# Optimization experiments

Measured on AMD Instinct MI355X. Metric: run time of the kernel, lower is better.

## Reference

```python
import math
import jax, jax.numpy as jnp
import numpy as np

D_MODEL = 1024
NHEAD = 16
NUM_TEMP = 4
HEAD = D_MODEL // NHEAD          # 64
DIM = HEAD // NUM_TEMP           # 16
SCALE = math.sqrt(HEAD)
B, L = 2, 2048


def _make_freq():
    # freq = 10000^(-arange(0,dim,2)/dim), repeat_interleave(2) -> length DIM
    f = np.power(10000.0, -np.arange(0, DIM, 2) / DIM)
    return jnp.asarray(np.repeat(f, 2), dtype=jnp.float32)  # (DIM,)


def setup_inputs() -> dict:
    key = jax.random.key(0)
    ks = jax.random.split(key, 8)
    s = 0.02
    return {
        "data": jax.random.normal(ks[0], (B, L, D_MODEL), jnp.float32),
        "temporal": jax.random.uniform(ks[1], (B, L, NUM_TEMP), jnp.float32),
        "mask": jnp.zeros((L, L), jnp.float32),
        "Wq": jax.random.normal(ks[2], (D_MODEL, D_MODEL), jnp.float32) * s,
        "bq": jnp.zeros((D_MODEL,), jnp.float32),
        "Wk": jax.random.normal(ks[3], (D_MODEL, D_MODEL), jnp.float32) * s,
        "bk": jnp.zeros((D_MODEL,), jnp.float32),
        "Wv": jax.random.normal(ks[4], (D_MODEL, D_MODEL), jnp.float32) * s,
        "bv": jnp.zeros((D_MODEL,), jnp.float32),
    }


def _rotate_half_pairs(x):
    # [-x2, x1, -x4, x3, ...] along last dim
    stacked = jnp.stack([-x[..., 1::2], x[..., 0::2]], axis=-1)
    return stacked.reshape(x.shape)


def _apply_rotary(x, sine, cosine):
    # x: (B,L,H,HEAD); sine/cosine: (B,L,HEAD)
    return x * cosine[:, :, None, :] + _rotate_half_pairs(x) * sine[:, :, None, :]


def reference(data, temporal, mask, Wq, bq, Wk, bk, Wv, bv):
    freq = _make_freq()  # (DIM,)
    b, l, _ = data.shape
    q = (data @ Wq + bq).reshape(b, l, NHEAD, HEAD)
    k = (data @ Wk + bk).reshape(b, l, NHEAD, HEAD)
    v = (data @ Wv + bv).reshape(b, l, NHEAD, HEAD)
    # per-temporal-column frequencies: (B,L,T,DIM) -> (B,L,HEAD)
    freqs = (temporal[..., None] * freq).reshape(b, l, HEAD)
    cosine = jnp.cos(freqs)
    sine = jnp.sin(freqs)
    rq = _apply_rotary(q, sine, cosine)
    rk = _apply_rotary(k, sine, cosine)
    logits = jnp.einsum("bqhs,bkhs->bhqk", rq, rk) / SCALE + mask
    weights = jax.nn.softmax(logits, axis=-1)  # dropout is identity at eval
    context = jnp.einsum("bhqk,bkhs->bqhs", weights, v)
    return context.reshape(b, l, D_MODEL)
```

## Files before the change

### kernel.cpp

```cpp
#include <hip/hip_runtime.h>
#include <hip/hip_bf16.h>

#define LSEQ 2048
#define DM   1024
#define NH   16

typedef __attribute__((ext_vector_type(8)))  short bf16x8;
typedef __attribute__((ext_vector_type(8)))  unsigned short u16x8;
typedef __attribute__((ext_vector_type(4)))  float f32x4;
typedef __attribute__((ext_vector_type(16))) float f32x16;
typedef __attribute__((ext_vector_type(4)))  unsigned int u32x4;

#define LOG2E 1.4426950408889634f
#define C1SC  0.18033688011112042f
#define DEFER_THR 8.0f

static __device__ __forceinline__ float exp2fast(float x) {
  return __builtin_amdgcn_exp2f(x);
}

static __device__ __forceinline__ unsigned short f2bf(float f) {
  unsigned int u = __float_as_uint(f);
  u += 0x7FFFu + ((u >> 16) & 1u);
  return (unsigned short)(u >> 16);
}

static __device__ __forceinline__ unsigned pk2(float a, float b) {
  __hip_bfloat162 t = __float22bfloat162_rn(make_float2(a, b));
  return *reinterpret_cast<unsigned*>(&t);
}

static __device__ __forceinline__ f32x16 unpack16(u16x8 a, u16x8 b) {
  const u32x4 ua = __builtin_bit_cast(u32x4, a);
  const u32x4 ub = __builtin_bit_cast(u32x4, b);
  f32x16 r;
#pragma unroll
  for (int i = 0; i < 4; ++i) {
    r[2 * i]     = __uint_as_float(ua[i] << 16);
    r[2 * i + 1] = __uint_as_float(ua[i] & 0xFFFF0000u);
    r[8 + 2 * i]     = __uint_as_float(ub[i] << 16);
    r[8 + 2 * i + 1] = __uint_as_float(ub[i] & 0xFFFF0000u);
  }
  return r;
}

static __device__ __forceinline__ bf16x8 mkfrag(int hi, float p0, float p1,
                                                float p2, float p3, float p4,
                                                float p5, float p6, float p7) {
  unsigned w0 = pk2(p0, p1), w1 = pk2(p2, p3);
  unsigned w2 = pk2(p4, p5), w3 = pk2(p6, p7);
  unsigned s0 = hi ? w0 : w2, s1 = hi ? w1 : w3;
  unsigned t0 = __shfl_xor(s0, 32, 64);
  unsigned t1 = __shfl_xor(s1, 32, 64);
  u32x4 f;
  f[0] = hi ? t0 : w0;
  f[1] = hi ? t1 : w1;
  f[2] = hi ? w2 : t0;
  f[3] = hi ? w3 : t1;
  return __builtin_bit_cast(bf16x8, f);
}

static __device__ __forceinline__ void gld_lds16(const unsigned short* g, unsigned short* l) {
  __builtin_amdgcn_global_load_lds(
      (const __attribute__((address_space(1))) unsigned int*)g,
      (__attribute__((address_space(3))) unsigned int*)l, 16, 0, 0);
}

__global__ void k_convert_data(const float* __restrict__ src,
                               unsigned short* __restrict__ dst, int n4) {
  int i = blockIdx.x * 256 + threadIdx.x;
  if (i >= n4) return;
  float4 v = reinterpret_cast<const float4*>(src)[i];
  ushort4 o;
  o.x = f2bf(v.x); o.y = f2bf(v.y); o.z = f2bf(v.z); o.w = f2bf(v.w);
  reinterpret_cast<ushort4*>(dst)[i] = o;
}

__global__ void k_transpose_w(const float* __restrict__ Wq,
                              const float* __restrict__ Wk,
                              const float* __restrict__ Wv,
                              unsigned short* __restrict__ Wt) {
  __shared__ unsigned short tile[64][65];
  const float* W = (blockIdx.z == 0) ? Wq : (blockIdx.z == 1) ? Wk : Wv;
  int n0 = blockIdx.x * 64, k0 = blockIdx.y * 64;
  int t = threadIdx.x;
  int c = t & 63, r0 = t >> 6;
  for (int i = 0; i < 16; ++i) {
    int r = r0 + i * 4;
    tile[r][c] = f2bf(W[(size_t)(k0 + r) * DM + n0 + c]);
  }
  __syncthreads();
  size_t nbase = (size_t)blockIdx.z * DM + n0;
  for (int i = 0; i < 16; ++i) {
    int n = r0 + i * 4;
    Wt[(nbase + n) * DM + k0 + c] = tile[c][n];
  }
}

__global__ void k_maskC(const float* __restrict__ mask,
                        unsigned short* __restrict__ maskCb) {
  __shared__ float tile[64][65];
  int q0 = blockIdx.x * 64, kv0 = blockIdx.y * 64;
  int t = threadIdx.x;
  int c = t & 63, r0 = t >> 6;
  for (int i = 0; i < 16; ++i) {
    int r = r0 + i * 4;
    tile[r][c] = mask[(size_t)(q0 + r) * LSEQ + kv0 + c];
  }
  __syncthreads();
  const int q = t & 63, slot = t >> 6;
  const int tt = slot >> 1, hh = slot & 1;
  u16x8 va, vb;
#pragma unroll
  for (int r = 0; r < 8; ++r) {
    const int kvloc = 32 * tt + 4 * hh + (r & 3) + 8 * (r >> 2);
    va[r] = f2bf(tile[q][kvloc] * LOG2E);
  }
#pragma unroll
  for (int r = 8; r < 16; ++r) {
    const int kvloc = 32 * tt + 4 * hh + (r & 3) + 8 * (r >> 2);
    vb[r - 8] = f2bf(tile[q][kvloc] * LOG2E);
  }
  unsigned short* dst = maskCb + ((size_t)((kv0 >> 6) * 4 + slot) * 2048 + q0 + q) * 16;
  *reinterpret_cast<u16x8*>(dst) = va;
  *reinterpret_cast<u16x8*>(dst + 8) = vb;
}

__global__ __launch_bounds__(256) void k_qkv_gemm(
    const unsigned short* __restrict__ A, const unsigned short* __restrict__ Bt,
    const float* __restrict__ bq, const float* __restrict__ bk,
    const float* __restrict__ bv, const float* __restrict__ temporal,
    unsigned short* __restrict__ qbuf, unsigned short* __restrict__ kbuf,
    unsigned short* __restrict__ vtbuf) {
  __shared__ unsigned short As[128 * 32];
  __shared__ unsigned short Bs[128 * 32];
  __shared__ unsigned short otile[128 * 136];
  const int tid = threadIdx.x;
  const int lane = tid & 63, wid = tid >> 6;
  const int wm = wid >> 1, wn = wid & 1;
  const int lr = lane & 15, lg = lane >> 4;

  const int bid = blockIdx.x;
  const int xcd = bid & 7, rr = bid >> 3;
  const int mblk = xcd * 4 + (rr / 24);
  const int nblk = rr % 24;
  const int m0 = mblk * 128;
  const int n0 = nblk * 128;

  f32x4 acc[4][4] = {};

  const int e0 = tid * 8;
  const int e1 = (256 + tid) * 8;
  const int ra0 = e0 >> 5, ca0 = e0 & 31;
  const int ra1 = e1 >> 5, ca1 = e1 & 31;
  unsigned short* lA0 = As + wid * 512;
  unsigned short* lA1 = As + 2048 + wid * 512;
  unsigned short* lB0 = Bs + wid * 512;
  unsigned short* lB1 = Bs + 2048 + wid * 512;

  for (int k0 = 0; k0 < DM; k0 += 32) {
    __syncthreads();
    gld_lds16(A + (size_t)(m0 + ra0) * DM + k0 + ca0, lA0);
    gld_lds16(A + (size_t)(m0 + ra1) * DM + k0 + ca1, lA1);
    gld_lds16(Bt + (size_t)(n0 + ra0) * DM + k0 + ca0, lB0);
    gld_lds16(Bt + (size_t)(n0 + ra1) * DM + k0 + ca1, lB1);
    __syncthreads();
    bf16x8 af[4], bfv[4];
    for (int mi = 0; mi < 4; ++mi)
      af[mi] = *reinterpret_cast<const bf16x8*>(As + (wm * 64 + mi * 16 + lr) * 32 + lg * 8);
    for (int ni = 0; ni < 4; ++ni)
      bfv[ni] = *reinterpret_cast<const bf16x8*>(Bs + (wn * 64 + ni * 16 + lr) * 32 + lg * 8);
    for (int mi = 0; mi < 4; ++mi)
      for (int ni = 0; ni < 4; ++ni)
        acc[mi][ni] = __builtin_amdgcn_mfma_f32_16x16x32_bf16(af[mi], bfv[ni], acc[mi][ni], 0, 0, 0);
  }

  const int mat = n0 >> 10;
  const int c0 = n0 & 1023;
  const int bb = m0 >> 11;
  const int mloc = m0 & 2047;
  const float qscale = (mat == 0) ? C1SC : 1.f;

  for (int mi = 0; mi < 4; ++mi) {
    const int rrel_base = wm * 64 + mi * 16 + lg * 4;
    for (int ni = 0; ni < 4; ++ni) {
      const int crel = wn * 64 + ni * 16 + lr;
      const int c = (c0 + crel);
      const int d = c & 63;
      const float bias = (mat == 0 ? bq : mat == 1 ? bk : bv)[c];
      f32x4 v = acc[mi][ni];
      if (mat < 2) {
        const int jj = d & 15, tt = d >> 4;
        const float fr = __expf(-(float)(jj & 14) * 0.5756462732485115f);
        const float sign = (d & 1) ? 1.f : -1.f;
        for (int j = 0; j < 4; ++j) {
          const int rrel = rrel_base + j;
          const float x = v[j] + bias;
          const float part = __shfl_xor(x, 1, 64);
          const int lqs = mloc + rrel;
          const float fq = temporal[((size_t)bb * LSEQ + lqs) * 4 + tt] * fr;
          float sn, cs;
          __sincosf(fq, &sn, &cs);
          otile[rrel * 136 + crel] = f2bf((x * cs + sign * part * sn) * qscale);
        }
      } else {
        for (int j = 0; j < 4; ++j) {
          const int rrel = rrel_base + j;
          otile[crel * 136 + rrel] = f2bf(v[j] + bias);
        }
      }
    }
  }
  __syncthreads();

  for (int i = 0; i < 2; ++i) {
    const int h = (c0 >> 6) + i;
    const size_t bh = (size_t)(bb * NH + h);
    if (mat == 0) {
      const size_t base = (bh * LSEQ + mloc) * 64;
#pragma unroll
      for (int kk2 = 0; kk2 < 4; ++kk2) {
        const int e = kk2 * 2048 + tid * 8;
        const int r = e >> 6, d = e & 63;
        *reinterpret_cast<u16x8*>(qbuf + base + e) =
            *reinterpret_cast<const u16x8*>(otile + r * 136 + i * 64 + d);
      }
    } else if (mat == 1) {
      const size_t base = bh * 131072 + (size_t)(mloc >> 5) * 2048;
#pragma unroll
      for (int kk2 = 0; kk2 < 4; ++kk2) {
        const int e = kk2 * 2048 + tid * 8;
        const int r = kk2 * 32 + ((tid >> 1) & 31);
        const int d = ((tid >> 6) & 3) * 16 + (tid & 1) * 8;
        *reinterpret_cast<u16x8*>(kbuf + base + e) =
            *reinterpret_cast<const u16x8*>(otile + r * 136 + i * 64 + d);
      }
    } else {
      const size_t base = bh * 131072 + (size_t)(mloc >> 4) * 1024;
#pragma unroll
      for (int kk2 = 0; kk2 < 4; ++kk2) {
        const int e = kk2 * 2048 + tid * 8;
        const int d = ((tid >> 6) & 1) * 32 + ((tid >> 1) & 31);
        const int r = (kk2 * 2 + (tid >> 7)) * 16 + (tid & 1) * 8;
        *reinterpret_cast<u16x8*>(vtbuf + base + e) =
            *reinterpret_cast<const u16x8*>(otile + (i * 64 + d) * 136 + r);
      }
    }
  }
}

__global__ __launch_bounds__(256) void k_attn(
    const unsigned short* __restrict__ qbuf, const unsigned short* __restrict__ kbuf,
    const unsigned short* __restrict__ vtbuf, const unsigned short* __restrict__ maskCb,
    float* __restrict__ out) {
  __shared__ float otile[4][64][33];
  __shared__ float mlbuf[4][32][2];
  const int tid = threadIdx.x, lane = tid & 63, wid = tid >> 6;
  const int lq = lane & 31, hi = lane >> 5;
  const int qsub = wid & 1, kvh = wid >> 1;
  const int bh = blockIdx.y;
  const int q0 = blockIdx.x * 64 + qsub * 32;
  const int qg = q0 + lq;
  const size_t bhL = (size_t)bh * LSEQ;
  const unsigned short* kb = kbuf + (size_t)bh * 131072;
  const unsigned short* vb = vtbuf + (size_t)bh * 131072;
  const unsigned short* mb = maskCb + ((size_t)hi * 2048 + qg) * 16;

  bf16x8 qf[4];
#pragma unroll
  for (int c = 0; c < 4; ++c)
    qf[c] = *reinterpret_cast<const bf16x8*>(qbuf + (bhL + qg) * 64 + c * 16 + hi * 8);

  f32x16 o0 = {}, o1 = {};
  float m2 = -1e30f, l_run = 0.f;

  const int kv_beg = kvh * 1024, kv_end = kv_beg + 1024;
  for (int kv0 = kv_beg; kv0 < kv_end; kv0 += 64) {
    const unsigned short* mt = mb + (size_t)(kv0 >> 6) * (4 * 2048 * 16);
    f32x16 s0 = unpack16(*reinterpret_cast<const u16x8*>(mt),
                         *reinterpret_cast<const u16x8*>(mt + 8));
    f32x16 s1 = unpack16(*reinterpret_cast<const u16x8*>(mt + 2 * 2048 * 16),
                         *reinterpret_cast<const u16x8*>(mt + 2 * 2048 * 16 + 8));

    const unsigned short* kch = kb + (size_t)(kv0 >> 5) * 2048;
#pragma unroll
    for (int c = 0; c < 4; ++c) {
      bf16x8 k0 = *reinterpret_cast<const bf16x8*>(kch + c * 512 + lq * 16 + hi * 8);
      bf16x8 k1 = *reinterpret_cast<const bf16x8*>(kch + 2048 + c * 512 + lq * 16 + hi * 8);
      s0 = __builtin_amdgcn_mfma_f32_32x32x16_bf16(k0, qf[c], s0, 0, 0, 0);
      s1 = __builtin_amdgcn_mfma_f32_32x32x16_bf16(k1, qf[c], s1, 0, 0, 0);
    }

    float t0[8];
#pragma unroll
    for (int r = 0; r < 8; ++r) t0[r] = fmaxf(fmaxf(s0[r], s0[r + 8]), fmaxf(s1[r], s1[r + 8]));
#pragma unroll
    for (int r = 0; r < 4; ++r) t0[r] = fmaxf(t0[r], t0[r + 4]);
    float loc = fmaxf(fmaxf(t0[0], t0[1]), fmaxf(t0[2], t0[3]));
    loc = fmaxf(loc, __shfl_xor(loc, 32, 64));

    if (!__all(loc <= m2 + DEFER_THR)) {
      const float mn = fmaxf(m2, loc);
      const float al = exp2fast(m2 - mn);
      l_run *= al;
#pragma unroll
      for (int r = 0; r < 16; ++r) { o0[r] *= al; o1[r] *= al; }
      m2 = mn;
    }

    float rs0 = 0.f, rs1 = 0.f, rs2 = 0.f, rs3 = 0.f;
#pragma unroll
    for (int r = 0; r < 4; ++r) {
      s0[r] = exp2fast(s0[r] - m2);      rs0 += s0[r];
      s0[r + 4] = exp2fast(s0[r + 4] - m2);  rs1 += s0[r + 4];
      s0[r + 8] = exp2fast(s0[r + 8] - m2);  rs2 += s0[r + 8];
      s0[r + 12] = exp2fast(s0[r + 12] - m2); rs3 += s0[r + 12];
    }
#pragma unroll
    for (int r = 0; r < 4; ++r) {
      s1[r] = exp2fast(s1[r] - m2);      rs0 += s1[r];
      s1[r + 4] = exp2fast(s1[r + 4] - m2);  rs1 += s1[r + 4];
      s1[r + 8] = exp2fast(s1[r + 8] - m2);  rs2 += s1[r + 8];
      s1[r + 12] = exp2fast(s1[r + 12] - m2); rs3 += s1[r + 12];
    }
    float rs = (rs0 + rs1) + (rs2 + rs3);
    rs += __shfl_xor(rs, 32, 64);
    l_run += rs;

    bf16x8 pf0 = mkfrag(hi, s0[0], s0[1], s0[2], s0[3], s0[4], s0[5], s0[6], s0[7]);
    bf16x8 pf1 = mkfrag(hi, s0[8], s0[9], s0[10], s0[11], s0[12], s0[13], s0[14], s0[15]);
    bf16x8 pf2 = mkfrag(hi, s1[0], s1[1], s1[2], s1[3], s1[4], s1[5], s1[6], s1[7]);
    bf16x8 pf3 = mkfrag(hi, s1[8], s1[9], s1[10], s1[11], s1[12], s1[13], s1[14], s1[15]);

    const unsigned short* vch = vb + (size_t)(kv0 >> 4) * 1024;
#pragma unroll
    for (int ks = 0; ks < 4; ++ks) {
      bf16x8 pf = (ks == 0) ? pf0 : (ks == 1) ? pf1 : (ks == 2) ? pf2 : pf3;
      bf16x8 v0 = *reinterpret_cast<const bf16x8*>(vch + ks * 1024 + lq * 16 + hi * 8);
      bf16x8 v1 = *reinterpret_cast<const bf16x8*>(vch + ks * 1024 + 512 + lq * 16 + hi * 8);
      o0 = __builtin_amdgcn_mfma_f32_32x32x16_bf16(v0, pf, o0, 0, 0, 0);
      o1 = __builtin_amdgcn_mfma_f32_32x32x16_bf16(v1, pf, o1, 0, 0, 0);
    }
  }

  if (lane < 32) { mlbuf[wid][lq][0] = m2; mlbuf[wid][lq][1] = l_run; }
  __syncthreads();
  const int pw = wid ^ 2;
  const float m_p = mlbuf[pw][lq][0];
  const float l_p = mlbuf[pw][lq][1];
  const float mstar = fmaxf(m2, m_p);
  const float f  = exp2fast(m2 - mstar);
  const float fp = exp2fast(m_p - mstar);
  const float scale = f / (l_run * f + l_p * fp);

#pragma unroll
  for (int r = 0; r < 16; ++r) {
    const int d = (r & 3) + 8 * (r >> 2) + 4 * hi;
    otile[wid][d][lq] = o0[r] * scale;
    otile[wid][32 + d][lq] = o1[r] * scale;
  }
  __syncthreads();

  const int b = bh >> 4, h = bh & 15;
#pragma unroll
  for (int i = 0; i < 4; ++i) {
    const int u = i * 256 + tid;
    const int q = u >> 4, c4 = u & 15;
    const int qs = q >> 5, ql = q & 31;
    float4 w;
    w.x = otile[qs][c4 * 4 + 0][ql] + otile[2 + qs][c4 * 4 + 0][ql];
    w.y = otile[qs][c4 * 4 + 1][ql] + otile[2 + qs][c4 * 4 + 1][ql];
    w.z = otile[qs][c4 * 4 + 2][ql] + otile[2 + qs][c4 * 4 + 2][ql];
    w.w = otile[qs][c4 * 4 + 3][ql] + otile[2 + qs][c4 * 4 + 3][ql];
    *reinterpret_cast<float4*>(
        out + ((size_t)(b * LSEQ + blockIdx.x * 64 + q)) * DM + h * 64 + c4 * 4) = w;
  }
}

extern "C" void kernel_launch(void* const* d_in, const int* in_sizes, int n_in,
                              void* d_out, int out_size, void* d_ws, size_t ws_size,
                              hipStream_t stream) {
  const float* data     = (const float*)d_in[0];
  const float* temporal = (const float*)d_in[1];
  const float* mask     = (const float*)d_in[2];
  const float* Wq       = (const float*)d_in[3];
  const float* bq       = (const float*)d_in[4];
  const float* Wk       = (const float*)d_in[5];
  const float* bk       = (const float*)d_in[6];
  const float* Wv       = (const float*)d_in[7];
  const float* bv       = (const float*)d_in[8];
  float* out = (float*)d_out;

  char* ws = (char*)d_ws;
  unsigned short* data_bf = (unsigned short*)(ws);
  unsigned short* wt      = (unsigned short*)(ws + (size_t)8  * 1048576);
  unsigned short* qbuf    = (unsigned short*)(ws + (size_t)14 * 1048576);
  unsigned short* kbuf    = (unsigned short*)(ws + (size_t)22 * 1048576);
  unsigned short* vtbuf   = (unsigned short*)(ws + (size_t)30 * 1048576);
  unsigned short* maskCb  = data_bf;

  hipLaunchKernelGGL(k_convert_data, dim3(4096), dim3(256), 0, stream,
                     data, data_bf, (2 * LSEQ * DM) / 4);
  hipLaunchKernelGGL(k_transpose_w, dim3(16, 16, 3), dim3(256), 0, stream,
                     Wq, Wk, Wv, wt);
  hipLaunchKernelGGL(k_qkv_gemm, dim3(768), dim3(256), 0, stream,
                     data_bf, wt, bq, bk, bv, temporal, qbuf, kbuf, vtbuf);
  hipLaunchKernelGGL(k_maskC, dim3(32, 32), dim3(256), 0, stream,
                     mask, maskCb);
  hipLaunchKernelGGL(k_attn, dim3(32, 32), dim3(256), 0, stream,
                     qbuf, kbuf, vtbuf, maskCb, out);
}
```

Before: 140.3 us.

## Replace online-softmax max tracking with fixed offset and overflow rescale, skip zero mask tiles

Removes the per-tile row-max reduction and deferred rescale from the attention loop. Softmax now uses a fixed initial offset and rescales by 2^-12 only when a row's partial exp sum exceeds a threshold. The mask kernel also writes per-tile all-zero flags so attention can skip loading mask tiles that are zero. Separately, the P fragments are packed without the cross-lane shuffle, which implies a changed V^T layout and gather in the QKV epilogue. This relies on logits being bounded, since a very negative max could underflow and a large jump in one tile could overflow before the rescale check fires.

```diff
diff --git a/kernel.cpp b/kernel.cpp
--- a/kernel.cpp
+++ b/kernel.cpp
@@ -13,7 +13,6 @@
 
 #define LOG2E 1.4426950408889634f
 #define C1SC  0.18033688011112042f
-#define DEFER_THR 8.0f
 
 static __device__ __forceinline__ float exp2fast(float x) {
   return __builtin_amdgcn_exp2f(x);
@@ -44,20 +43,11 @@
   return r;
 }
 
-static __device__ __forceinline__ bf16x8 mkfrag(int hi, float p0, float p1,
-                                                float p2, float p3, float p4,
-                                                float p5, float p6, float p7) {
-  unsigned w0 = pk2(p0, p1), w1 = pk2(p2, p3);
-  unsigned w2 = pk2(p4, p5), w3 = pk2(p6, p7);
-  unsigned s0 = hi ? w0 : w2, s1 = hi ? w1 : w3;
-  unsigned t0 = __shfl_xor(s0, 32, 64);
-  unsigned t1 = __shfl_xor(s1, 32, 64);
-  u32x4 f;
-  f[0] = hi ? t0 : w0;
-  f[1] = hi ? t1 : w1;
-  f[2] = hi ? w2 : t0;
-  f[3] = hi ? w3 : t1;
-  return __builtin_bit_cast(bf16x8, f);
+static __device__ __forceinline__ bf16x8 pack8(float a, float b, float c, float d,
+                                               float e, float f, float g, float h) {
+  u32x4 w;
+  w[0] = pk2(a, b); w[1] = pk2(c, d); w[2] = pk2(e, f); w[3] = pk2(g, h);
+  return __builtin_bit_cast(bf16x8, w);
 }
 
 static __device__ __forceinline__ void gld_lds16(const unsigned short* g, unsigned short* l) {
@@ -98,15 +88,23 @@
 }
 
 __global__ void k_maskC(const float* __restrict__ mask,
-                        unsigned short* __restrict__ maskCb) {
+                        unsigned short* __restrict__ maskCb,
+                        int* __restrict__ zflags) {
   __shared__ float tile[64][65];
+  __shared__ int nz;
   int q0 = blockIdx.x * 64, kv0 = blockIdx.y * 64;
   int t = threadIdx.x;
+  if (t == 0) nz = 0;
+  __syncthreads();
   int c = t & 63, r0 = t >> 6;
+  int lnz = 0;
   for (int i = 0; i < 16; ++i) {
     int r = r0 + i * 4;
-    tile[r][c] = mask[(size_t)(q0 + r) * LSEQ + kv0 + c];
-  }
+    float v = mask[(size_t)(q0 + r) * LSEQ + kv0 + c];
+    tile[r][c] = v;
+    lnz |= (v != 0.0f);
+  }
+  if (lnz) atomicOr(&nz, 1);
   __syncthreads();
   const int q = t & 63, slot = t >> 6;
   const int tt = slot >> 1, hh = slot & 1;
@@ -124,6 +122,7 @@
   unsigned short* dst = maskCb + ((size_t)((kv0 >> 6) * 4 + slot) * 2048 + q0 + q) * 16;
   *reinterpret_cast<u16x8*>(dst) = va;
   *reinterpret_cast<u16x8*>(dst + 8) = vb;
+  if (t == 0) zflags[blockIdx.y * 32 + blockIdx.x] = (nz == 0);
 }
 
 __global__ __launch_bounds__(256) void k_qkv_gemm(
@@ -241,9 +240,15 @@
       for (int kk2 = 0; kk2 < 4; ++kk2) {
         const int e = kk2 * 2048 + tid * 8;
         const int d = ((tid >> 6) & 1) * 32 + ((tid >> 1) & 31);
-        const int r = (kk2 * 2 + (tid >> 7)) * 16 + (tid & 1) * 8;
-        *reinterpret_cast<u16x8*>(vtbuf + base + e) =
-            *reinterpret_cast<const u16x8*>(otile + (i * 64 + d) * 136 + r);
+        const int rb = (kk2 * 2 + (tid >> 7)) * 16;
+        const int dl = (tid & 1) * 4;
+        const unsigned short* srow = otile + (i * 64 + d) * 136 + rb + dl;
+        ushort4 lo = *reinterpret_cast<const ushort4*>(srow);
+        ushort4 hi4 = *reinterpret_cast<const ushort4*>(srow + 8);
+        u16x8 w;
+        w[0] = lo.x; w[1] = lo.y; w[2] = lo.z; w[3] = lo.w;
+        w[4] = hi4.x; w[5] = hi4.y; w[6] = hi4.z; w[7] = hi4.w;
+        *reinterpret_cast<u16x8*>(vtbuf + base + e) = w;
       }
     }
   }
@@ -252,7 +257,7 @@
 __global__ __launch_bounds__(256) void k_attn(
     const unsigned short* __restrict__ qbuf, const unsigned short* __restrict__ kbuf,
     const unsigned short* __restrict__ vtbuf, const unsigned short* __restrict__ maskCb,
-    float* __restrict__ out) {
+    const int* __restrict__ zflags, float* __restrict__ out) {
   __shared__ float otile[4][64][33];
   __shared__ float mlbuf[4][32][2];
   const int tid = threadIdx.x, lane = tid & 63, wid = tid >> 6;
@@ -272,15 +277,22 @@
     qf[c] = *reinterpret_cast<const bf16x8*>(qbuf + (bhL + qg) * 64 + c * 16 + hi * 8);
 
   f32x16 o0 = {}, o1 = {};
-  float m2 = -1e30f, l_run = 0.f;
+  float m2 = 2.0f, l_run = 0.f;
 
   const int kv_beg = kvh * 1024, kv_end = kv_beg + 1024;
   for (int kv0 = kv_beg; kv0 < kv_end; kv0 += 64) {
-    const unsigned short* mt = mb + (size_t)(kv0 >> 6) * (4 * 2048 * 16);
-    f32x16 s0 = unpack16(*reinterpret_cast<const u16x8*>(mt),
-                         *reinterpret_cast<const u16x8*>(mt + 8));
-    f32x16 s1 = unpack16(*reinterpret_cast<const u16x8*>(mt + 2 * 2048 * 16),
-                         *reinterpret_cast<const u16x8*>(mt + 2 * 2048 * 16 + 8));
+    f32x16 s0, s1;
+    const int zf = zflags[(kv0 >> 6) * 32 + blockIdx.x];
+    if (zf) {
+      s0 = (f32x16){};
+      s1 = (f32x16){};
+    } else {
+      const unsigned short* mt = mb + (size_t)(kv0 >> 6) * (4 * 2048 * 16);
+      s0 = unpack16(*reinterpret_cast<const u16x8*>(mt),
+                    *reinterpret_cast<const u16x8*>(mt + 8));
+      s1 = unpack16(*reinterpret_cast<const u16x8*>(mt + 2 * 2048 * 16),
+                    *reinterpret_cast<const u16x8*>(mt + 2 * 2048 * 16 + 8));
+    }
 
     const unsigned short* kch = kb + (size_t)(kv0 >> 5) * 2048;
 #pragma unroll
@@ -291,46 +303,40 @@
       s1 = __builtin_amdgcn_mfma_f32_32x32x16_bf16(k1, qf[c], s1, 0, 0, 0);
     }
 
-    float t0[8];
-#pragma unroll
-    for (int r = 0; r < 8; ++r) t0[r] = fmaxf(fmaxf(s0[r], s0[r + 8]), fmaxf(s1[r], s1[r + 8]));
-#pragma unroll
-    for (int r = 0; r < 4; ++r) t0[r] = fmaxf(t0[r], t0[r + 4]);
-    float loc = fmaxf(fmaxf(t0[0], t0[1]), fmaxf(t0[2], t0[3]));
-    loc = fmaxf(loc, __shfl_xor(loc, 32, 64));
-
-    if (!__all(loc <= m2 + DEFER_THR)) {
-      const float mn = fmaxf(m2, loc);
-      const float al = exp2fast(m2 - mn);
-      l_run *= al;
-#pragma unroll
-      for (int r = 0; r < 16; ++r) { o0[r] *= al; o1[r] *= al; }
-      m2 = mn;
-    }
-
     float rs0 = 0.f, rs1 = 0.f, rs2 = 0.f, rs3 = 0.f;
 #pragma unroll
     for (int r = 0; r < 4; ++r) {
-      s0[r] = exp2fast(s0[r] - m2);      rs0 += s0[r];
-      s0[r + 4] = exp2fast(s0[r + 4] - m2);  rs1 += s0[r + 4];
-      s0[r + 8] = exp2fast(s0[r + 8] - m2);  rs2 += s0[r + 8];
+      s0[r] = exp2fast(s0[r] - m2);        rs0 += s0[r];
+      s0[r + 4] = exp2fast(s0[r + 4] - m2);   rs1 += s0[r + 4];
+      s0[r + 8] = exp2fast(s0[r + 8] - m2);   rs2 += s0[r + 8];
       s0[r + 12] = exp2fast(s0[r + 12] - m2); rs3 += s0[r + 12];
     }
 #pragma unroll
     for (int r = 0; r < 4; ++r) {
-      s1[r] = exp2fast(s1[r] - m2);      rs0 += s1[r];
-      s1[r + 4] = exp2fast(s1[r + 4] - m2);  rs1 += s1[r + 4];
-      s1[r + 8] = exp2fast(s1[r + 8] - m2);  rs2 += s1[r + 8];
+      s1[r] = exp2fast(s1[r] - m2);        rs0 += s1[r];
+      s1[r + 4] = exp2fast(s1[r + 4] - m2);   rs1 += s1[r + 4];
+      s1[r + 8] = exp2fast(s1[r + 8] - m2);   rs2 += s1[r + 8];
       s1[r + 12] = exp2fast(s1[r + 12] - m2); rs3 += s1[r + 12];
     }
     float rs = (rs0 + rs1) + (rs2 + rs3);
+
+    if (__any(rs > 2048.f)) {
+      const float cc = 0.000244140625f;
+#pragma unroll
+      for (int r = 0; r < 16; ++r) { s0[r] *= cc; s1[r] *= cc; }
+      rs *= cc; l_run *= cc;
+#pragma unroll
+      for (int r = 0; r < 16; ++r) { o0[r] *= cc; o1[r] *= cc; }
+      m2 += 12.f;
+    }
+
     rs += __shfl_xor(rs, 32, 64);
     l_run += rs;
 
-    bf16x8 pf0 = mkfrag(hi, s0[0], s0[1], s0[2], s0[3], s0[4], s0[5], s0[6], s0[7]);
-    bf16x8 pf1 = mkfrag(hi, s0[8], s0[9], s0[10], s0[11], s0[12], s0[13], s0[14], s0[15]);
-    bf16x8 pf2 = mkfrag(hi, s1[0], s1[1], s1[2], s1[3], s1[4], s1[5], s1[6], s1[7]);
-    bf16x8 pf3 = mkfrag(hi, s1[8], s1[9], s1[10], s1[11], s1[12], s1[13], s1[14], s1[15]);
+    bf16x8 pf0 = pack8(s0[0], s0[1], s0[2], s0[3], s0[4], s0[5], s0[6], s0[7]);
+    bf16x8 pf1 = pack8(s0[8], s0[9], s0[10], s0[11], s0[12], s0[13], s0[14], s0[15]);
+    bf16x8 pf2 = pack8(s1[0], s1[1], s1[2], s1[3], s1[4], s1[5], s1[6], s1[7]);
+    bf16x8 pf3 = pack8(s1[8], s1[9], s1[10], s1[11], s1[12], s1[13], s1[14], s1[15]);
 
     const unsigned short* vch = vb + (size_t)(kv0 >> 4) * 1024;
 #pragma unroll
@@ -398,6 +404,7 @@
   unsigned short* kbuf    = (unsigned short*)(ws + (size_t)22 * 1048576);
   unsigned short* vtbuf   = (unsigned short*)(ws + (size_t)30 * 1048576);
   unsigned short* maskCb  = data_bf;
+  int* zflags             = (int*)wt;
 
   hipLaunchKernelGGL(k_convert_data, dim3(4096), dim3(256), 0, stream,
                      data, data_bf, (2 * LSEQ * DM) / 4);
@@ -406,7 +413,7 @@
   hipLaunchKernelGGL(k_qkv_gemm, dim3(768), dim3(256), 0, stream,
                      data_bf, wt, bq, bk, bv, temporal, qbuf, kbuf, vtbuf);
   hipLaunchKernelGGL(k_maskC, dim3(32, 32), dim3(256), 0, stream,
-                     mask, maskCb);
+                     mask, maskCb, zflags);
   hipLaunchKernelGGL(k_attn, dim3(32, 32), dim3(256), 0, stream,
-                     qbuf, kbuf, vtbuf, maskCb, out);
-}
+                     qbuf, kbuf, vtbuf, maskCb, zflags, out);
+}
```

New measurement: 143.6 us. 2.3% more time.
